# Performance work log

Hardware: AMD Instinct MI355X
Metric: run time of the kernel (lower is better)

Reference implementation:

```python
import jax, jax.numpy as jnp
import numpy as np

B, T, D_IN, EMB, H = 2, 2048, 1024, 1024, 16
HD = EMB // H  # head_dim = 64


def setup_inputs() -> dict:
    key = jax.random.key(0)
    ks = jax.random.split(key, 3)
    scale_qkv = 1.0 / np.sqrt(D_IN)
    scale_o = 1.0 / np.sqrt(EMB)
    return {
        "x": jax.random.normal(ks[0], (B, T, D_IN), dtype=jnp.float32),
        "W_qkv": jax.random.normal(ks[1], (D_IN, 3 * EMB), dtype=jnp.float32) * scale_qkv,
        "b_qkv": jnp.zeros((3 * EMB,), dtype=jnp.float32),
        "W_o": jax.random.normal(ks[2], (EMB, EMB), dtype=jnp.float32) * scale_o,
        "b_o": jnp.zeros((EMB,), dtype=jnp.float32),
    }


def reference(x, W_qkv, b_qkv, W_o, b_o):
    b, t, _ = x.shape
    qkv = x @ W_qkv + b_qkv                      # [B,T,3*EMB]
    # Match torch: reshape to (B,T,H,3*HD) -> permute -> chunk into q,k,v
    qkv = qkv.reshape(b, t, H, 3 * HD).transpose(0, 2, 1, 3)  # [B,H,T,3*HD]
    q, k, v = jnp.split(qkv, 3, axis=-1)         # each [B,H,T,HD]
    scale = 1.0 / jnp.sqrt(jnp.asarray(HD, dtype=q.dtype))
    scores = jnp.einsum("bhqd,bhkd->bhqk", q, k) * scale  # [B,H,T,T]
    attn = jax.nn.softmax(scores, axis=-1)
    values = jnp.einsum("bhqk,bhkd->bhqd", attn, v)       # [B,H,T,HD]
    values = values.transpose(0, 2, 1, 3).reshape(b, t, EMB)
    return values @ W_o + b_o
```

## Files before the change

kernel.cpp:

```cpp
#include <hip/hip_runtime.h>
#include <math.h>

typedef __bf16 bf16x8 __attribute__((ext_vector_type(8)));
typedef float f32x4 __attribute__((ext_vector_type(4)));
typedef short s16x4 __attribute__((ext_vector_type(4)));

#define GPTR(p) ((const __attribute__((address_space(1))) void*)(p))
#define LPTR(p) ((__attribute__((address_space(3))) void*)(p))

#define QSCALE 0.18033688011112042f

__device__ __forceinline__ unsigned short f2bf(float f) {
  unsigned int u = __float_as_uint(f);
  u += 0x7FFFu + ((u >> 16) & 1u);
  return (unsigned short)(u >> 16);
}

__device__ __forceinline__ unsigned int pack_bf2(float lo, float hi) {
  return __builtin_amdgcn_perm(__float_as_uint(hi) + 0x8000u,
                               __float_as_uint(lo) + 0x8000u, 0x07060302u);
}

__device__ __forceinline__ float fast_exp2(float x) {
#if __has_builtin(__builtin_amdgcn_exp2f)
  return __builtin_amdgcn_exp2f(x);
#else
  return exp2f(x);
#endif
}

__device__ __forceinline__ f32x4 zero4() {
  f32x4 z; z[0] = 0.f; z[1] = 0.f; z[2] = 0.f; z[3] = 0.f; return z;
}

__global__ void conv_x_bf16(const float* __restrict__ in, unsigned short* __restrict__ out) {
  int i = (blockIdx.x * 256 + threadIdx.x) * 4;
  float4 v = *(const float4*)(in + i);
  ushort4 o;
  o.x = f2bf(v.x); o.y = f2bf(v.y); o.z = f2bf(v.z); o.w = f2bf(v.w);
  *(ushort4*)(out + i) = o;
}

__global__ void transpose_conv(const float* __restrict__ in, unsigned short* __restrict__ out,
                               int K, int N) {
  __shared__ float tile[64][65];
  int k0 = blockIdx.y * 64, n0 = blockIdx.x * 64;
  int t = threadIdx.x;
#pragma unroll
  for (int p = 0; p < 16; ++p) {
    int l = p * 256 + t; int r = l >> 6, c = l & 63;
    tile[r][c] = in[(size_t)(k0 + r) * N + n0 + c];
  }
  __syncthreads();
#pragma unroll
  for (int p = 0; p < 16; ++p) {
    int l = p * 256 + t; int r = l >> 6, c = l & 63;
    out[(size_t)(n0 + r) * K + k0 + c] = f2bf(tile[c][r]);
  }
}

__global__ __launch_bounds__(256) void gemm_qkv(
    const unsigned short* __restrict__ A, const unsigned short* __restrict__ Bt,
    const float* __restrict__ bias,
    unsigned short* __restrict__ Qd, unsigned short* __restrict__ Kd,
    unsigned short* __restrict__ Vtd) {
  __shared__ unsigned short As[128 * 32];
  __shared__ unsigned short Bs[128 * 32];
  const int tid = threadIdx.x, wave = tid >> 6, lane = tid & 63;
  const int quad = lane >> 4, l16 = lane & 15;
  const int wm = (wave >> 1) * 64, wn = (wave & 1) * 64;
  const int m0 = blockIdx.y * 128, n0 = blockIdx.x * 128;
  f32x4 acc[4][4];
#pragma unroll
  for (int i = 0; i < 4; ++i)
#pragma unroll
    for (int j = 0; j < 4; ++j) acc[i][j] = zero4();

  const int c = wave * 64 + lane;
  const int rA = c >> 2, o16 = (c & 3) * 8;

  for (int k0 = 0; k0 < 1024; k0 += 32) {
    __syncthreads();
    __builtin_amdgcn_global_load_lds(GPTR(A + (size_t)(m0 + rA) * 1024 + k0 + o16),
                                     LPTR(As + wave * 512), 16, 0, 0);
    __builtin_amdgcn_global_load_lds(GPTR(A + (size_t)(m0 + 64 + rA) * 1024 + k0 + o16),
                                     LPTR(As + 2048 + wave * 512), 16, 0, 0);
    __builtin_amdgcn_global_load_lds(GPTR(Bt + (size_t)(n0 + rA) * 1024 + k0 + o16),
                                     LPTR(Bs + wave * 512), 16, 0, 0);
    __builtin_amdgcn_global_load_lds(GPTR(Bt + (size_t)(n0 + 64 + rA) * 1024 + k0 + o16),
                                     LPTR(Bs + 2048 + wave * 512), 16, 0, 0);
    __syncthreads();
    bf16x8 af[4], bfr[4];
#pragma unroll
    for (int mt = 0; mt < 4; ++mt)
      af[mt] = *(const bf16x8*)(As + (wm + mt * 16 + l16) * 32 + quad * 8);
#pragma unroll
    for (int nt = 0; nt < 4; ++nt)
      bfr[nt] = *(const bf16x8*)(Bs + (wn + nt * 16 + l16) * 32 + quad * 8);
#pragma unroll
    for (int mt = 0; mt < 4; ++mt)
#pragma unroll
      for (int nt = 0; nt < 4; ++nt)
        acc[mt][nt] = __builtin_amdgcn_mfma_f32_16x16x32_bf16(af[mt], bfr[nt], acc[mt][nt], 0, 0, 0);
  }

#pragma unroll
  for (int mt = 0; mt < 4; ++mt) {
#pragma unroll
    for (int nt = 0; nt < 4; ++nt) {
      int m = m0 + wm + mt * 16 + quad * 4;
      int n = n0 + wn + nt * 16 + l16;
      float bv = bias[n];
      int h = n / 192, rem = n - h * 192;
      int which = rem >> 6, d = rem & 63;
      int b = m >> 11, t0 = m & 2047;
      size_t head = (size_t)(b * 16 + h);
      f32x4 a = acc[mt][nt];
      if (which == 0) {
        size_t base = (head * 2048 + t0) * 64 + d;
#pragma unroll
        for (int i = 0; i < 4; ++i)
          Qd[base + (size_t)i * 64] = f2bf((a[i] + bv) * QSCALE);
      } else if (which == 1) {
        size_t base = head * 131072 + (size_t)(t0 >> 6) * 4096;
#pragma unroll
        for (int i = 0; i < 4; ++i) {
          int tt = t0 + i;
          Kd[base + (tt & 63) * 64 + (((d >> 3) ^ (tt & 7)) << 3) + (d & 7)] = f2bf(a[i] + bv);
        }
      } else {
        size_t base = head * 131072 + (size_t)(t0 >> 6) * 4096;
        ushort4 o;
        o.x = f2bf(a[0] + bv); o.y = f2bf(a[1] + bv);
        o.z = f2bf(a[2] + bv); o.w = f2bf(a[3] + bv);
        *(ushort4*)(Vtd + base + d * 64 + (((((t0 & 63) >> 3)) ^ (d & 7)) << 3) + (t0 & 7)) = o;
      }
    }
  }
}

__global__ __launch_bounds__(256) void flash_attn(
    const unsigned short* __restrict__ Qg,
    const unsigned short* __restrict__ Kg,
    const unsigned short* __restrict__ Vg,
    unsigned short* __restrict__ att) {
  __shared__ __align__(16) char smem[33792];
  unsigned short* Ks = (unsigned short*)smem;
  unsigned short* Vs = Ks + 4096;
  float* redO = (float*)smem;
  float* redL = (float*)(smem + 32768);
  const int tid = threadIdx.x, wave = tid >> 6, lane = tid & 63;
  const int quad = lane >> 4, l16 = lane & 15;
  const int h7 = l16 & 7;
  const int qhalf = wave >> 1, kh2 = wave & 1;
  const int bh = blockIdx.y;
  const int q0 = blockIdx.x * 128 + qhalf * 64;

  bf16x8 bq[4][2];
#pragma unroll
  for (int qg = 0; qg < 4; ++qg)
#pragma unroll
    for (int kh = 0; kh < 2; ++kh)
      bq[qg][kh] = *(const bf16x8*)(Qg + ((size_t)bh * 2048 + q0 + qg * 16 + l16) * 64 + kh * 32 + quad * 8);

  f32x4 o[4][4];
#pragma unroll
  for (int mt = 0; mt < 4; ++mt)
#pragma unroll
    for (int qg = 0; qg < 4; ++qg) o[mt][qg] = zero4();
  float lacc[4] = {0.f, 0.f, 0.f, 0.f};

  const unsigned short* Kt = Kg + (size_t)bh * 131072;
  const unsigned short* Vt = Vg + (size_t)bh * 131072;

  for (int tile = 0; tile < 32; ++tile) {
    __syncthreads();
    const unsigned short* Kb = Kt + tile * 4096 + lane * 8;
    const unsigned short* Vb = Vt + tile * 4096 + lane * 8;
    __builtin_amdgcn_global_load_lds(GPTR(Kb + wave * 512),       LPTR(Ks + wave * 512), 16, 0, 0);
    __builtin_amdgcn_global_load_lds(GPTR(Kb + (4 + wave) * 512), LPTR(Ks + (4 + wave) * 512), 16, 0, 0);
    __builtin_amdgcn_global_load_lds(GPTR(Vb + wave * 512),       LPTR(Vs + wave * 512), 16, 0, 0);
    __builtin_amdgcn_global_load_lds(GPTR(Vb + (4 + wave) * 512), LPTR(Vs + (4 + wave) * 512), 16, 0, 0);
    __syncthreads();

    f32x4 s[4][2];
#pragma unroll
    for (int qg = 0; qg < 4; ++qg)
#pragma unroll
      for (int kt = 0; kt < 2; ++kt) s[qg][kt] = zero4();
#pragma unroll
    for (int kt = 0; kt < 2; ++kt) {
      int krow = kh2 * 32 + kt * 16 + l16;
#pragma unroll
      for (int kh = 0; kh < 2; ++kh) {
        bf16x8 a = *(const bf16x8*)(Ks + krow * 64 + (((kh * 4 + quad) ^ h7) << 3));
#pragma unroll
        for (int qg = 0; qg < 4; ++qg)
          s[qg][kt] = __builtin_amdgcn_mfma_f32_16x16x32_bf16(a, bq[qg][kh], s[qg][kt], 0, 0, 0);
      }
    }

#pragma unroll
    for (int kt = 0; kt < 2; ++kt) {
      s16x4 pB[4];
#pragma unroll
      for (int qg = 0; qg < 4; ++qg) {
        float p0 = fast_exp2(s[qg][kt][0]);
        float p1 = fast_exp2(s[qg][kt][1]);
        float p2 = fast_exp2(s[qg][kt][2]);
        float p3 = fast_exp2(s[qg][kt][3]);
        lacc[qg] += (p0 + p1) + (p2 + p3);
        union { unsigned int u[2]; s16x4 v; } pk;
        pk.u[0] = pack_bf2(p0, p1);
        pk.u[1] = pack_bf2(p2, p3);
        pB[qg] = pk.v;
      }
      int cV = kh2 * 4 + kt * 2 + (quad >> 1);
#pragma unroll
      for (int mt = 0; mt < 4; ++mt) {
        s16x4 aV = *(const s16x4*)(Vs + (mt * 16 + l16) * 64 + ((cV ^ h7) << 3) + (quad & 1) * 4);
#pragma unroll
        for (int qg = 0; qg < 4; ++qg)
          o[mt][qg] = __builtin_amdgcn_mfma_f32_16x16x16bf16_1k(aV, pB[qg], o[mt][qg], 0, 0, 0);
      }
    }
  }

  float lfull[4];
#pragma unroll
  for (int qg = 0; qg < 4; ++qg) {
    float lw = lacc[qg];
    lw += __shfl_xor(lw, 16);
    lw += __shfl_xor(lw, 32);
    lfull[qg] = lw;
  }
  __syncthreads();
  if (kh2 == 1) {
    float* ob = redO + qhalf * 4096;
#pragma unroll
    for (int mt = 0; mt < 4; ++mt)
#pragma unroll
      for (int qg = 0; qg < 4; ++qg)
        *(f32x4*)(ob + ((qg * 4 + mt) * 4 + quad) * 64 + l16 * 4) = o[mt][qg];
    if (quad == 0) {
#pragma unroll
      for (int qg = 0; qg < 4; ++qg)
        redL[qhalf * 64 + qg * 16 + l16] = lfull[qg];
    }
  }
  __syncthreads();
  if (kh2 == 0) {
    int b = bh >> 4, h = bh & 15;
    float* ob = redO + qhalf * 4096;
#pragma unroll
    for (int qg = 0; qg < 4; ++qg) {
      float linv = 1.f / (lfull[qg] + redL[qhalf * 64 + qg * 16 + l16]);
      unsigned short* orow = att + ((size_t)b * 2048 + q0 + qg * 16 + l16) * 1024 + h * 64;
#pragma unroll
      for (int mt = 0; mt < 4; ++mt) {
        f32x4 part = *(const f32x4*)(ob + ((qg * 4 + mt) * 4 + quad) * 64 + l16 * 4);
        ushort4 ov;
        ov.x = f2bf((o[mt][qg][0] + part[0]) * linv);
        ov.y = f2bf((o[mt][qg][1] + part[1]) * linv);
        ov.z = f2bf((o[mt][qg][2] + part[2]) * linv);
        ov.w = f2bf((o[mt][qg][3] + part[3]) * linv);
        *(ushort4*)(orow + mt * 16 + quad * 4) = ov;
      }
    }
  }
}

__global__ __launch_bounds__(256) void gemm_out(
    const unsigned short* __restrict__ A, const unsigned short* __restrict__ Bt,
    const float* __restrict__ bias, float* __restrict__ out) {
  __shared__ unsigned short As[128 * 32];
  __shared__ unsigned short Bs[128 * 32];
  const int tid = threadIdx.x, wave = tid >> 6, lane = tid & 63;
  const int quad = lane >> 4, l16 = lane & 15;
  const int wm = (wave >> 1) * 64, wn = (wave & 1) * 64;
  const int m0 = blockIdx.y * 128, n0 = blockIdx.x * 128;
  f32x4 acc[4][4];
#pragma unroll
  for (int i = 0; i < 4; ++i)
#pragma unroll
    for (int j = 0; j < 4; ++j) acc[i][j] = zero4();

  const int c = wave * 64 + lane;
  const int rA = c >> 2, o16 = (c & 3) * 8;

  for (int k0 = 0; k0 < 1024; k0 += 32) {
    __syncthreads();
    __builtin_amdgcn_global_load_lds(GPTR(A + (size_t)(m0 + rA) * 1024 + k0 + o16),
                                     LPTR(As + wave * 512), 16, 0, 0);
    __builtin_amdgcn_global_load_lds(GPTR(A + (size_t)(m0 + 64 + rA) * 1024 + k0 + o16),
                                     LPTR(As + 2048 + wave * 512), 16, 0, 0);
    __builtin_amdgcn_global_load_lds(GPTR(Bt + (size_t)(n0 + rA) * 1024 + k0 + o16),
                                     LPTR(Bs + wave * 512), 16, 0, 0);
    __builtin_amdgcn_global_load_lds(GPTR(Bt + (size_t)(n0 + 64 + rA) * 1024 + k0 + o16),
                                     LPTR(Bs + 2048 + wave * 512), 16, 0, 0);
    __syncthreads();
    bf16x8 af[4], bfr[4];
#pragma unroll
    for (int mt = 0; mt < 4; ++mt)
      af[mt] = *(const bf16x8*)(As + (wm + mt * 16 + l16) * 32 + quad * 8);
#pragma unroll
    for (int nt = 0; nt < 4; ++nt)
      bfr[nt] = *(const bf16x8*)(Bs + (wn + nt * 16 + l16) * 32 + quad * 8);
#pragma unroll
    for (int mt = 0; mt < 4; ++mt)
#pragma unroll
      for (int nt = 0; nt < 4; ++nt)
        acc[mt][nt] = __builtin_amdgcn_mfma_f32_16x16x32_bf16(af[mt], bfr[nt], acc[mt][nt], 0, 0, 0);
  }

#pragma unroll
  for (int mt = 0; mt < 4; ++mt) {
#pragma unroll
    for (int nt = 0; nt < 4; ++nt) {
      int m = m0 + wm + mt * 16 + quad * 4;
      int n = n0 + wn + nt * 16 + l16;
      float bv = bias[n];
      float* orow = out + (size_t)m * 1024 + n;
      orow[0]        = acc[mt][nt][0] + bv;
      orow[1024]     = acc[mt][nt][1] + bv;
      orow[2 * 1024] = acc[mt][nt][2] + bv;
      orow[3 * 1024] = acc[mt][nt][3] + bv;
    }
  }
}

extern "C" void kernel_launch(void* const* d_in, const int* in_sizes, int n_in,
                              void* d_out, int out_size, void* d_ws, size_t ws_size,
                              hipStream_t stream) {
  const float* x    = (const float*)d_in[0];
  const float* Wqkv = (const float*)d_in[1];
  const float* bqkv = (const float*)d_in[2];
  const float* Wo   = (const float*)d_in[3];
  const float* bo   = (const float*)d_in[4];
  float* out = (float*)d_out;

  unsigned short* xb    = (unsigned short*)d_ws;
  unsigned short* wqkvt = xb    + (size_t)4096 * 1024;
  unsigned short* wot   = wqkvt + (size_t)3072 * 1024;
  unsigned short* Qd    = wot   + (size_t)1024 * 1024;
  unsigned short* Kd    = Qd    + (size_t)32 * 2048 * 64;
  unsigned short* Vtd   = Kd    + (size_t)32 * 2048 * 64;
  unsigned short* attb  = Vtd   + (size_t)32 * 2048 * 64;

  conv_x_bf16<<<4096, 256, 0, stream>>>(x, xb);
  transpose_conv<<<dim3(48, 16), 256, 0, stream>>>(Wqkv, wqkvt, 1024, 3072);
  transpose_conv<<<dim3(16, 16), 256, 0, stream>>>(Wo, wot, 1024, 1024);
  gemm_qkv<<<dim3(24, 32), 256, 0, stream>>>(xb, wqkvt, bqkv, Qd, Kd, Vtd);
  flash_attn<<<dim3(16, 32), 256, 0, stream>>>(Qd, Kd, Vtd, attb);
  gemm_out<<<dim3(8, 32), 256, 0, stream>>>(attb, wot, bo, out);
}
```

Before: 222.5 us.

## Double-buffer K/V tiles in LDS to overlap loads with attention compute

The flash attention loop now keeps two LDS buffers for the K/V tiles. It prefetches tile t+1 with global_load_lds while tile t is computed, which removes the second barrier from each iteration. This is meant to hide global-to-LDS latency behind the MFMA and softmax work. It uses the full 32 KB LDS region and relies on the single top-of-loop barrier to wait for the in-flight loads and to order buffer reuse.

```diff
diff --git a/kernel.cpp b/kernel.cpp
--- a/kernel.cpp
+++ b/kernel.cpp
@@ -145,8 +145,7 @@
     const unsigned short* __restrict__ Vg,
     unsigned short* __restrict__ att) {
   __shared__ __align__(16) char smem[33792];
-  unsigned short* Ks = (unsigned short*)smem;
-  unsigned short* Vs = Ks + 4096;
+  unsigned short* Tb = (unsigned short*)smem;
   float* redO = (float*)smem;
   float* redL = (float*)(smem + 32768);
   const int tid = threadIdx.x, wave = tid >> 6, lane = tid & 63;
@@ -170,18 +169,30 @@
     for (int qg = 0; qg < 4; ++qg) o[mt][qg] = zero4();
   float lacc[4] = {0.f, 0.f, 0.f, 0.f};
 
-  const unsigned short* Kt = Kg + (size_t)bh * 131072;
-  const unsigned short* Vt = Vg + (size_t)bh * 131072;
+  const unsigned short* Kt = Kg + (size_t)bh * 131072 + lane * 8;
+  const unsigned short* Vt = Vg + (size_t)bh * 131072 + lane * 8;
+
+  {
+    unsigned short* Kb = Tb;
+    __builtin_amdgcn_global_load_lds(GPTR(Kt + wave * 512),          LPTR(Kb + wave * 512), 16, 0, 0);
+    __builtin_amdgcn_global_load_lds(GPTR(Kt + (4 + wave) * 512),    LPTR(Kb + (4 + wave) * 512), 16, 0, 0);
+    __builtin_amdgcn_global_load_lds(GPTR(Vt + wave * 512),          LPTR(Kb + 4096 + wave * 512), 16, 0, 0);
+    __builtin_amdgcn_global_load_lds(GPTR(Vt + (4 + wave) * 512),    LPTR(Kb + 4096 + (4 + wave) * 512), 16, 0, 0);
+  }
 
   for (int tile = 0; tile < 32; ++tile) {
     __syncthreads();
-    const unsigned short* Kb = Kt + tile * 4096 + lane * 8;
-    const unsigned short* Vb = Vt + tile * 4096 + lane * 8;
-    __builtin_amdgcn_global_load_lds(GPTR(Kb + wave * 512),       LPTR(Ks + wave * 512), 16, 0, 0);
-    __builtin_amdgcn_global_load_lds(GPTR(Kb + (4 + wave) * 512), LPTR(Ks + (4 + wave) * 512), 16, 0, 0);
-    __builtin_amdgcn_global_load_lds(GPTR(Vb + wave * 512),       LPTR(Vs + wave * 512), 16, 0, 0);
-    __builtin_amdgcn_global_load_lds(GPTR(Vb + (4 + wave) * 512), LPTR(Vs + (4 + wave) * 512), 16, 0, 0);
-    __syncthreads();
+    if (tile + 1 < 32) {
+      unsigned short* Kb = Tb + ((tile + 1) & 1) * 8192;
+      const unsigned short* Kg1 = Kt + (tile + 1) * 4096;
+      const unsigned short* Vg1 = Vt + (tile + 1) * 4096;
+      __builtin_amdgcn_global_load_lds(GPTR(Kg1 + wave * 512),       LPTR(Kb + wave * 512), 16, 0, 0);
+      __builtin_amdgcn_global_load_lds(GPTR(Kg1 + (4 + wave) * 512), LPTR(Kb + (4 + wave) * 512), 16, 0, 0);
+      __builtin_amdgcn_global_load_lds(GPTR(Vg1 + wave * 512),       LPTR(Kb + 4096 + wave * 512), 16, 0, 0);
+      __builtin_amdgcn_global_load_lds(GPTR(Vg1 + (4 + wave) * 512), LPTR(Kb + 4096 + (4 + wave) * 512), 16, 0, 0);
+    }
+    const unsigned short* Ks = Tb + (tile & 1) * 8192;
+    const unsigned short* Vs = Ks + 4096;
 
     f32x4 s[4][2];
 #pragma unroll
```

Result: no change. 219.9 us (-1.2%).
